# Performance work log

Measured on AMD Instinct MI355X. Metric: run time of the kernel, lower is better.

## Reference

```python
import jax, jax.numpy as jnp
import numpy as np

RETURN_SHAPE = (128, 128)


def dht2(x):
    # Discrete Hartley Transform over the spatial axes (2, 3):
    # H = Re(FFT) - Im(FFT). Unnormalized, matching scipy.fft default.
    f = jnp.fft.fftn(x, axes=(2, 3))
    return f.real - f.imag


def setup_inputs() -> dict:
    key = jax.random.key(0)
    x = jax.random.normal(key, (8, 64, 256, 256), dtype=jnp.float32)
    return {"x": x}


def reference(x) -> jnp.ndarray:
    # Spectral pooling: DHT -> center crop in frequency domain -> DHT.
    h_out, w_out = RETURN_SHAPE
    H, W = x.shape[2], x.shape[3]
    d = dht2(x)
    sh = (H - h_out) // 2
    sw = (W - w_out) // 2
    cropped = d[:, :, sh:sh + h_out, sw:sw + w_out]
    return dht2(cropped).astype(jnp.float32)
```

## Files before the change

kernel.cpp:

```cpp
#include <hip/hip_runtime.h>
#include <math.h>


typedef __attribute__((ext_vector_type(8))) short bfrag;
typedef __attribute__((ext_vector_type(4))) float ffrag;

#define PI2_256 0.0245436926061702597f
#define PI2_128 0.0490873852123405194f

__device__ __forceinline__ unsigned short f2bf(float f) {
    union { float f; unsigned int u; } v; v.f = f;
    unsigned int r = v.u + 0x7fffu + ((v.u >> 16) & 1u);
    return (unsigned short)(r >> 16);
}

__device__ __forceinline__ bfrag pack8(float4 a, float4 b) {
    bfrag r;
    r[0] = (short)f2bf(a.x); r[1] = (short)f2bf(a.y);
    r[2] = (short)f2bf(a.z); r[3] = (short)f2bf(a.w);
    r[4] = (short)f2bf(b.x); r[5] = (short)f2bf(b.y);
    r[6] = (short)f2bf(b.z); r[7] = (short)f2bf(b.w);
    return r;
}

__device__ __forceinline__ uint2 packlohi(ffrag a) {
    uint2 r;
    r.x = (unsigned int)f2bf(a[0]) | ((unsigned int)f2bf(a[1]) << 16);
    r.y = (unsigned int)f2bf(a[2]) | ((unsigned int)f2bf(a[3]) << 16);
    return r;
}

template<int NCOLS, int K, int NTH>
__device__ __forceinline__ void stageB(const unsigned short* __restrict__ src,
                                       unsigned short* __restrict__ Lb, int t)
{
    constexpr int CHUNKS = NCOLS * K / 8;
#pragma unroll
    for (int i = 0; i < CHUNKS / NTH; ++i) {
        const int o = (t + i * NTH) * 8;
        const int j = o / K;
        const int k = o - j * K;
        const uint4 v = *(const uint4*)(src + o);
        *(uint4*)&Lb[j * K + (((k >> 3) ^ (j & 7)) << 3)] = v;
    }
}

template<int K>
__device__ __forceinline__ bfrag ldsB(const unsigned short* __restrict__ Lb, int j, int k)
{
    return *(const bfrag*)&Lb[j * K + (((k >> 3) ^ (j & 7)) << 3)];
}

__global__ __launch_bounds__(256) void gen_tables(unsigned short* __restrict__ ws)
{
    const int id = blockIdx.x * 256 + threadIdx.x;
    {
        const int j = id >> 8, m = id & 255;
        const int mult = (j < 128) ? (64 + j) : (320 - j);
        const int idx = (mult * m) & 255;
        float s, c; sincosf((float)idx * PI2_256, &s, &c);
        ws[id] = f2bf(c + s);
    }
    {
        const int u = id >> 9, k = id & 511;
        const int up = 64 + u;
        float s, c, val;
        if (k < 256) { sincosf((float)((up * k) & 255) * PI2_256, &s, &c); val = c; }
        else         { sincosf((float)((up * (k - 256)) & 255) * PI2_256, &s, &c); val = s; }
        ws[65536 + id] = f2bf(val);
    }
    if (id < 32768) {
        {
            const int j = id >> 7, m = id & 127;
            const int mult = (j < 128) ? j : (256 - j);
            const int idx = (mult * m) & 127;
            float s, c; sincosf((float)idx * PI2_128, &s, &c);
            ws[131072 + id] = f2bf(c + s);
        }
        {
            const int u = id >> 8, k = id & 255;
            float s, c, val;
            if (k < 128) { sincosf((float)((u * k) & 127) * PI2_128, &s, &c); val = c; }
            else         { sincosf((float)((u * (k - 128)) & 127) * PI2_128, &s, &c); val = s; }
            ws[163840 + id] = f2bf(val);
        }
    }
}

__global__ __launch_bounds__(256, 1) void pass1(const float* __restrict__ X,
                                                const unsigned short* __restrict__ ws,
                                                unsigned short* __restrict__ Ct)
{
    __shared__ unsigned short Lb[128 * 256];

    const int t  = threadIdx.x;
    const int w  = t >> 6;
    const int ln = t & 15;
    const int q  = (t & 63) >> 4;
    const int img = blockIdx.x >> 1;
    const int h   = blockIdx.x & 1;

    stageB<128, 256, 256>(ws + h * 32768, Lb, t);
    __syncthreads();

    const float* __restrict__ Xi = X + (size_t)img * 65536;

    ffrag acc[4][8];
#pragma unroll
    for (int mt = 0; mt < 4; ++mt)
#pragma unroll
        for (int nt = 0; nt < 8; ++nt)
            acc[mt][nt] = (ffrag){0.f, 0.f, 0.f, 0.f};

#pragma unroll
    for (int kk = 0; kk < 8; ++kk) {
        const int k = kk * 32 + q * 8;
        bfrag A[4];
#pragma unroll
        for (int mt = 0; mt < 4; ++mt) {
            const float* xp = Xi + (size_t)(64 * w + 16 * mt + ln) * 256 + k;
            const float4 x0 = *(const float4*)xp;
            const float4 x1 = *(const float4*)(xp + 4);
            A[mt] = pack8(x0, x1);
        }
#pragma unroll
        for (int nt = 0; nt < 8; ++nt) {
            const bfrag B = ldsB<256>(Lb, nt * 16 + ln, k);
#pragma unroll
            for (int mt = 0; mt < 4; ++mt)
                acc[mt][nt] = __builtin_amdgcn_mfma_f32_16x16x32_bf16(A[mt], B, acc[mt][nt], 0, 0, 0);
        }
    }
#pragma unroll
    for (int mt = 0; mt < 4; ++mt) {
        unsigned short* __restrict__ Co = Ct + (size_t)img * 65536 + 64 * w + 16 * mt + 4 * q;
#pragma unroll
        for (int nt = 0; nt < 8; ++nt) {
            *(uint2*)&Co[(size_t)(128 * h + nt * 16 + ln) * 256] = packlohi(acc[mt][nt]);
        }
    }
}

__global__ __launch_bounds__(256, 2) void pass2(const unsigned short* __restrict__ Ct,
                                                const unsigned short* __restrict__ ws,
                                                unsigned short* __restrict__ Dc)
{
    __shared__ unsigned short Lb[64 * 512];

    const int t  = threadIdx.x;
    const int w  = t >> 6;
    const int ln = t & 15;
    const int q  = (t & 63) >> 4;
    const int img = blockIdx.x >> 1;
    const int hu  = blockIdx.x & 1;

    stageB<64, 512, 256>(ws + 65536 + hu * 32768, Lb, t);
    __syncthreads();

    const unsigned short* __restrict__ Abase = Ct + (size_t)img * 65536;

    ffrag acc[2][4];
#pragma unroll
    for (int mt = 0; mt < 2; ++mt)
#pragma unroll
        for (int nt = 0; nt < 4; ++nt)
            acc[mt][nt] = (ffrag){0.f, 0.f, 0.f, 0.f};

#pragma unroll
    for (int kh = 0; kh < 2; ++kh) {
#pragma unroll
        for (int kk = 0; kk < 8; ++kk) {
            const int k = kk * 32 + q * 8;
            const int kfull = kh * 256 + k;
            bfrag A[2];
#pragma unroll
            for (int mt = 0; mt < 2; ++mt) {
                const int v = 32 * w + 16 * mt + ln;
                A[mt] = *(const bfrag*)(Abase + (size_t)(v + kh * 128) * 256 + k);
            }
#pragma unroll
            for (int nt = 0; nt < 4; ++nt) {
                const bfrag B = ldsB<512>(Lb, nt * 16 + ln, kfull);
#pragma unroll
                for (int mt = 0; mt < 2; ++mt)
                    acc[mt][nt] = __builtin_amdgcn_mfma_f32_16x16x32_bf16(A[mt], B, acc[mt][nt], 0, 0, 0);
            }
        }
    }
#pragma unroll
    for (int mt = 0; mt < 2; ++mt) {
        unsigned short* __restrict__ Do = Dc + (size_t)img * 16384 + 32 * w + 16 * mt + 4 * q;
#pragma unroll
        for (int nt = 0; nt < 4; ++nt) {
            *(uint2*)&Do[(size_t)(64 * hu + nt * 16 + ln) * 128] = packlohi(acc[mt][nt]);
        }
    }
}

__global__ __launch_bounds__(256, 2) void pass3(const unsigned short* __restrict__ Dc,
                                                const unsigned short* __restrict__ ws,
                                                unsigned short* __restrict__ C3t)
{
    __shared__ unsigned short Lb[128 * 128];

    const int t  = threadIdx.x;
    const int w  = t >> 6;
    const int ln = t & 15;
    const int q  = (t & 63) >> 4;
    const int img = blockIdx.x >> 1;
    const int hj  = blockIdx.x & 1;

    stageB<128, 128, 256>(ws + 131072 + hj * 16384, Lb, t);
    __syncthreads();

    const unsigned short* __restrict__ Abase = Dc + (size_t)img * 16384;

    ffrag acc[2][8];
#pragma unroll
    for (int mt = 0; mt < 2; ++mt)
#pragma unroll
        for (int nt = 0; nt < 8; ++nt)
            acc[mt][nt] = (ffrag){0.f, 0.f, 0.f, 0.f};

#pragma unroll
    for (int kk = 0; kk < 4; ++kk) {
        const int k = kk * 32 + q * 8;
        bfrag A[2];
#pragma unroll
        for (int mt = 0; mt < 2; ++mt) {
            const int p = 32 * w + 16 * mt + ln;
            A[mt] = *(const bfrag*)(Abase + (size_t)p * 128 + k);
        }
#pragma unroll
        for (int nt = 0; nt < 8; ++nt) {
            const bfrag B = ldsB<128>(Lb, nt * 16 + ln, k);
#pragma unroll
            for (int mt = 0; mt < 2; ++mt)
                acc[mt][nt] = __builtin_amdgcn_mfma_f32_16x16x32_bf16(A[mt], B, acc[mt][nt], 0, 0, 0);
        }
    }
#pragma unroll
    for (int mt = 0; mt < 2; ++mt) {
        unsigned short* __restrict__ Co = C3t + (size_t)img * 32768 + 32 * w + 16 * mt + 4 * q;
#pragma unroll
        for (int nt = 0; nt < 8; ++nt) {
            *(uint2*)&Co[(size_t)(128 * hj + nt * 16 + ln) * 128] = packlohi(acc[mt][nt]);
        }
    }
}

__global__ __launch_bounds__(256, 2) void pass4(const unsigned short* __restrict__ C3t,
                                                const unsigned short* __restrict__ ws,
                                                float* __restrict__ out)
{
    __shared__ unsigned short Lb[64 * 256];

    const int t  = threadIdx.x;
    const int w  = t >> 6;
    const int ln = t & 15;
    const int q  = (t & 63) >> 4;
    const int img = blockIdx.x >> 1;
    const int hu  = blockIdx.x & 1;

    stageB<64, 256, 256>(ws + 163840 + hu * 16384, Lb, t);
    __syncthreads();

    const unsigned short* __restrict__ Abase = C3t + (size_t)img * 32768;

    ffrag acc[2][4];
#pragma unroll
    for (int mt = 0; mt < 2; ++mt)
#pragma unroll
        for (int nt = 0; nt < 4; ++nt)
            acc[mt][nt] = (ffrag){0.f, 0.f, 0.f, 0.f};

#pragma unroll
    for (int kh = 0; kh < 2; ++kh) {
#pragma unroll
        for (int kk = 0; kk < 4; ++kk) {
            const int k = kk * 32 + q * 8;
            const int kfull = kh * 128 + k;
            bfrag A[2];
#pragma unroll
            for (int mt = 0; mt < 2; ++mt) {
                const int v = 32 * w + 16 * mt + ln;
                A[mt] = *(const bfrag*)(Abase + (size_t)(v + kh * 128) * 128 + k);
            }
#pragma unroll
            for (int nt = 0; nt < 4; ++nt) {
                const bfrag B = ldsB<256>(Lb, nt * 16 + ln, kfull);
#pragma unroll
                for (int mt = 0; mt < 2; ++mt)
                    acc[mt][nt] = __builtin_amdgcn_mfma_f32_16x16x32_bf16(A[mt], B, acc[mt][nt], 0, 0, 0);
            }
        }
    }
#pragma unroll
    for (int mt = 0; mt < 2; ++mt) {
        float* __restrict__ G = out + (size_t)img * 16384 + 32 * w + 16 * mt + 4 * q;
#pragma unroll
        for (int nt = 0; nt < 4; ++nt) {
            float4 o4 = make_float4(acc[mt][nt][0], acc[mt][nt][1], acc[mt][nt][2], acc[mt][nt][3]);
            *(float4*)&G[(size_t)(64 * hu + nt * 16 + ln) * 128] = o4;
        }
    }
}

__global__ __launch_bounds__(512, 2) void stage1_old(const float* __restrict__ X,
                                                     const unsigned short* __restrict__ ws,
                                                     float* __restrict__ dc)
{
    __shared__ unsigned short PQt[128 * 512];

    const int t  = threadIdx.x;
    const int w  = t >> 6;
    const int ln = t & 15;
    const int q  = (t & 63) >> 4;
    const int img = blockIdx.x;

    const float* __restrict__ Xi = X + (size_t)img * 65536;
    const unsigned short* __restrict__ W1 = ws;
    const unsigned short* __restrict__ W2 = ws + 65536;

    {
        ffrag acc[2][16];
#pragma unroll
        for (int mt = 0; mt < 2; ++mt)
#pragma unroll
            for (int nt = 0; nt < 16; ++nt)
                acc[mt][nt] = (ffrag){0.f, 0.f, 0.f, 0.f};

        const int rowA0 = 32 * w;
        for (int kk = 0; kk < 8; ++kk) {
            const int k = kk * 32 + q * 8;
            bfrag A[2];
#pragma unroll
            for (int mt = 0; mt < 2; ++mt) {
                const float* xp = Xi + (size_t)(rowA0 + 16 * mt + ln) * 256 + k;
                const float4 x0 = *(const float4*)xp;
                const float4 x1 = *(const float4*)(xp + 4);
                A[mt] = pack8(x0, x1);
            }
#pragma unroll
            for (int nt = 0; nt < 16; ++nt) {
                const int j = nt * 16 + ln;
                const bfrag B = *(const bfrag*)(W1 + j * 256 + k);
#pragma unroll
                for (int mt = 0; mt < 2; ++mt)
                    acc[mt][nt] = __builtin_amdgcn_mfma_f32_16x16x32_bf16(A[mt], B, acc[mt][nt], 0, 0, 0);
            }
        }
#pragma unroll
        for (int mt = 0; mt < 2; ++mt) {
#pragma unroll
            for (int nt = 0; nt < 16; ++nt) {
                const int c  = nt * 16 + ln;
                const int v  = c & 127;
                const int kb = ((c < 128) ? 0 : 256) + rowA0 + 16 * mt + 4 * q;
                const uint2 lohi = packlohi(acc[mt][nt]);
                const int phys = v * 512 + (((kb >> 3) ^ (v & 7)) << 3) + (kb & 7);
                *(uint2*)&PQt[phys] = lohi;
            }
        }
    }
    __syncthreads();

    {
        ffrag acc[8];
#pragma unroll
        for (int nt = 0; nt < 8; ++nt) acc[nt] = (ffrag){0.f, 0.f, 0.f, 0.f};

        const int u0 = 16 * w;
        for (int kk = 0; kk < 16; ++kk) {
            const int k = kk * 32 + q * 8;
            const bfrag A = *(const bfrag*)(W2 + (size_t)(u0 + ln) * 512 + k);
#pragma unroll
            for (int nt = 0; nt < 8; ++nt) {
                const int v = nt * 16 + ln;
                const int g = (k >> 3) ^ (v & 7);
                const bfrag B = *(const bfrag*)&PQt[v * 512 + (g << 3)];
                acc[nt] = __builtin_amdgcn_mfma_f32_16x16x32_bf16(A, B, acc[nt], 0, 0, 0);
            }
        }
        float* __restrict__ D = dc + (size_t)img * 16384;
#pragma unroll
        for (int nt = 0; nt < 8; ++nt) {
#pragma unroll
            for (int r = 0; r < 4; ++r) {
                const int u = u0 + 4 * q + r;
                const int v = nt * 16 + ln;
                D[u * 128 + v] = acc[nt][r];
            }
        }
    }
}

__global__ __launch_bounds__(256, 2) void stage2_old(const unsigned short* __restrict__ ws,
                                                     float* __restrict__ io)
{
    __shared__ unsigned short Dcb[128 * 128];
    __shared__ unsigned short PQ2[64 * 256];

    const int t  = threadIdx.x;
    const int w  = t >> 6;
    const int ln = t & 15;
    const int q  = (t & 63) >> 4;
    const int img = blockIdx.x;

    float* __restrict__ G = io + (size_t)img * 16384;
    const unsigned short* __restrict__ W3 = ws + 131072;
    const unsigned short* __restrict__ W4 = ws + 163840;

    {
        const int p = t >> 1, half = t & 1;
        const float* src = G + p * 128 + half * 64;
#pragma unroll
        for (int g = 0; g < 8; ++g) {
            const float4 a = *(const float4*)(src + g * 8);
            const float4 b = *(const float4*)(src + g * 8 + 4);
            const int m0 = half * 64 + g * 8;
            const int gran = (m0 >> 3) ^ (p & 7);
            uint4 val;
            val.x = (unsigned int)f2bf(a.x) | ((unsigned int)f2bf(a.y) << 16);
            val.y = (unsigned int)f2bf(a.z) | ((unsigned int)f2bf(a.w) << 16);
            val.z = (unsigned int)f2bf(b.x) | ((unsigned int)f2bf(b.y) << 16);
            val.w = (unsigned int)f2bf(b.z) | ((unsigned int)f2bf(b.w) << 16);
            *(uint4*)&Dcb[p * 128 + gran * 8] = val;
        }
    }
    __syncthreads();

    for (int vh = 0; vh < 2; ++vh) {
        ffrag acc[2][8];
#pragma unroll
        for (int mt = 0; mt < 2; ++mt)
#pragma unroll
            for (int nt = 0; nt < 8; ++nt)
                acc[mt][nt] = (ffrag){0.f, 0.f, 0.f, 0.f};

        const int p0 = 32 * w;
        for (int kk = 0; kk < 4; ++kk) {
            const int k = kk * 32 + q * 8;
            bfrag A[2];
#pragma unroll
            for (int mt = 0; mt < 2; ++mt) {
                const int p = p0 + 16 * mt + ln;
                const int g = (k >> 3) ^ (p & 7);
                A[mt] = *(const bfrag*)&Dcb[p * 128 + g * 8];
            }
#pragma unroll
            for (int nt = 0; nt < 8; ++nt) {
                const int c = nt * 16 + ln;
                const int j = (c < 64) ? (64 * vh + c) : (128 + 64 * vh + (c - 64));
                const bfrag B = *(const bfrag*)(W3 + j * 128 + k);
#pragma unroll
                for (int mt = 0; mt < 2; ++mt)
                    acc[mt][nt] = __builtin_amdgcn_mfma_f32_16x16x32_bf16(A[mt], B, acc[mt][nt], 0, 0, 0);
            }
        }
        __syncthreads();
#pragma unroll
        for (int mt = 0; mt < 2; ++mt) {
#pragma unroll
            for (int nt = 0; nt < 8; ++nt) {
                const int c  = nt * 16 + ln;
                const int v  = c & 63;
                const int kb = ((c < 64) ? 0 : 128) + p0 + 16 * mt + 4 * q;
                const uint2 lohi = packlohi(acc[mt][nt]);
                const int phys = v * 256 + (((kb >> 3) ^ (v & 7)) << 3) + (kb & 7);
                *(uint2*)&PQ2[phys] = lohi;
            }
        }
        __syncthreads();

        ffrag o[2][4];
#pragma unroll
        for (int mt = 0; mt < 2; ++mt)
#pragma unroll
            for (int nt = 0; nt < 4; ++nt)
                o[mt][nt] = (ffrag){0.f, 0.f, 0.f, 0.f};

        const int u0 = 32 * w;
        for (int kk = 0; kk < 8; ++kk) {
            const int k = kk * 32 + q * 8;
            bfrag A[2];
#pragma unroll
            for (int mt = 0; mt < 2; ++mt)
                A[mt] = *(const bfrag*)(W4 + (size_t)(u0 + 16 * mt + ln) * 256 + k);
#pragma unroll
            for (int nt = 0; nt < 4; ++nt) {
                const int v = nt * 16 + ln;
                const int g = (k >> 3) ^ (v & 7);
                const bfrag B = *(const bfrag*)&PQ2[v * 256 + (g << 3)];
#pragma unroll
                for (int mt = 0; mt < 2; ++mt)
                    o[mt][nt] = __builtin_amdgcn_mfma_f32_16x16x32_bf16(A[mt], B, o[mt][nt], 0, 0, 0);
            }
        }
#pragma unroll
        for (int mt = 0; mt < 2; ++mt) {
#pragma unroll
            for (int nt = 0; nt < 4; ++nt) {
#pragma unroll
                for (int r = 0; r < 4; ++r) {
                    const int u = u0 + 16 * mt + 4 * q + r;
                    const int v = 64 * vh + nt * 16 + ln;
                    G[u * 128 + v] = o[mt][nt][r];
                }
            }
        }
    }
}

extern "C" void kernel_launch(void* const* d_in, const int* in_sizes, int n_in,
                              void* d_out, int out_size, void* d_ws, size_t ws_size,
                              hipStream_t stream)
{
    const float* x = (const float*)d_in[0];
    float* out = (float*)d_out;
    unsigned short* tw = (unsigned short*)d_ws;

    gen_tables<<<dim3(256), dim3(256), 0, stream>>>(tw);

    int G = 512;
    while (G > 1 && (size_t)163840 * (size_t)G + 393216 > ws_size) G >>= 1;

    if ((size_t)163840 * (size_t)G + 393216 <= ws_size) {
        unsigned short* regA  = tw + 196608;
        unsigned short* regDc = regA + (size_t)G * 65536;
        const int nchunks = 512 / G;
        for (int ci = 0; ci < nchunks; ++ci) {
            const float* xc = x + (size_t)ci * G * 65536;
            float* oc = out + (size_t)ci * G * 16384;
            pass1<<<dim3(2 * G), dim3(256), 0, stream>>>(xc, tw, regA);
            pass2<<<dim3(G * 2), dim3(256), 0, stream>>>(regA, tw, regDc);
            pass3<<<dim3(2 * G), dim3(256), 0, stream>>>(regDc, tw, regA);
            pass4<<<dim3(2 * G), dim3(256), 0, stream>>>(regA, tw, oc);
        }
    } else {
        stage1_old<<<dim3(512), dim3(512), 0, stream>>>(x, tw, out);
        stage2_old<<<dim3(512), dim3(256), 0, stream>>>(tw, out);
    }
}
```

Measured before the change: 289.1 us.

## Pre-convert input to bf16, split pass1 into quarter blocks, stage output via LDS

Adds a separate kernel that converts the fp32 input to bf16 once, so pass1 loads bf16 fragments directly instead of converting fp32 in its inner loop. pass1 now covers a quarter of the output columns per block with half the LDS, allowing two blocks per CU. Its results are transposed through swizzled LDS so the global stores are coalesced 16-byte writes. This costs an extra kernel launch plus a full bf16 write and read of the input, and the workspace requirement grows.

```diff
diff --git a/kernel.cpp b/kernel.cpp
--- a/kernel.cpp
+++ b/kernel.cpp
@@ -87,29 +87,42 @@
     }
 }
 
-__global__ __launch_bounds__(256, 1) void pass1(const float* __restrict__ X,
+__global__ __launch_bounds__(256) void convertX(const float* __restrict__ X,
+                                                unsigned short* __restrict__ Xb,
+                                                int n8)
+{
+    const int stride = gridDim.x * 256;
+    for (int i = blockIdx.x * 256 + threadIdx.x; i < n8; i += stride) {
+        const float4 a = *(const float4*)(X + (size_t)i * 8);
+        const float4 b = *(const float4*)(X + (size_t)i * 8 + 4);
+        const bfrag v = pack8(a, b);
+        *(uint4*)&Xb[(size_t)i * 8] = *(const uint4*)&v;
+    }
+}
+
+__global__ __launch_bounds__(256, 2) void pass1(const unsigned short* __restrict__ Xb,
                                                 const unsigned short* __restrict__ ws,
                                                 unsigned short* __restrict__ Ct)
 {
-    __shared__ unsigned short Lb[128 * 256];
+    __shared__ unsigned short Lb[64 * 256];
 
     const int t  = threadIdx.x;
     const int w  = t >> 6;
     const int ln = t & 15;
     const int q  = (t & 63) >> 4;
-    const int img = blockIdx.x >> 1;
-    const int h   = blockIdx.x & 1;
-
-    stageB<128, 256, 256>(ws + h * 32768, Lb, t);
-    __syncthreads();
-
-    const float* __restrict__ Xi = X + (size_t)img * 65536;
-
-    ffrag acc[4][8];
+    const int img = blockIdx.x >> 2;
+    const int h   = blockIdx.x & 3;
+
+    stageB<64, 256, 256>(ws + h * 16384, Lb, t);
+    __syncthreads();
+
+    const unsigned short* __restrict__ Xi = Xb + (size_t)img * 65536;
+
+    ffrag acc[4][4];
 #pragma unroll
     for (int mt = 0; mt < 4; ++mt)
 #pragma unroll
-        for (int nt = 0; nt < 8; ++nt)
+        for (int nt = 0; nt < 4; ++nt)
             acc[mt][nt] = (ffrag){0.f, 0.f, 0.f, 0.f};
 
 #pragma unroll
@@ -117,27 +130,37 @@
         const int k = kk * 32 + q * 8;
         bfrag A[4];
 #pragma unroll
-        for (int mt = 0; mt < 4; ++mt) {
-            const float* xp = Xi + (size_t)(64 * w + 16 * mt + ln) * 256 + k;
-            const float4 x0 = *(const float4*)xp;
-            const float4 x1 = *(const float4*)(xp + 4);
-            A[mt] = pack8(x0, x1);
-        }
-#pragma unroll
-        for (int nt = 0; nt < 8; ++nt) {
+        for (int mt = 0; mt < 4; ++mt)
+            A[mt] = *(const bfrag*)(Xi + (size_t)(64 * w + 16 * mt + ln) * 256 + k);
+#pragma unroll
+        for (int nt = 0; nt < 4; ++nt) {
             const bfrag B = ldsB<256>(Lb, nt * 16 + ln, k);
 #pragma unroll
             for (int mt = 0; mt < 4; ++mt)
                 acc[mt][nt] = __builtin_amdgcn_mfma_f32_16x16x32_bf16(A[mt], B, acc[mt][nt], 0, 0, 0);
         }
     }
+
+    __syncthreads();
 #pragma unroll
     for (int mt = 0; mt < 4; ++mt) {
-        unsigned short* __restrict__ Co = Ct + (size_t)img * 65536 + 64 * w + 16 * mt + 4 * q;
-#pragma unroll
-        for (int nt = 0; nt < 8; ++nt) {
-            *(uint2*)&Co[(size_t)(128 * h + nt * 16 + ln) * 256] = packlohi(acc[mt][nt]);
-        }
+#pragma unroll
+        for (int nt = 0; nt < 4; ++nt) {
+            const int cl = nt * 16 + ln;
+            const int n2 = 16 * w + 4 * mt + q;
+            const int phys = cl * 256 + (((n2 ^ ((cl & 7) << 3)) << 2));
+            *(uint2*)&Lb[phys] = packlohi(acc[mt][nt]);
+        }
+    }
+    __syncthreads();
+    unsigned short* __restrict__ Co = Ct + (size_t)img * 65536 + 16384 * h;
+#pragma unroll
+    for (int j = 0; j < 8; ++j) {
+        const int o   = (t + j * 256) * 8;
+        const int row = o >> 8;
+        const int ch  = (o & 255) >> 2;
+        const int phys = row * 256 + (((ch ^ ((row & 7) << 3)) << 2));
+        *(uint4*)&Co[o] = *(const uint4*)&Lb[phys];
     }
 }
 
@@ -523,18 +546,19 @@
     gen_tables<<<dim3(256), dim3(256), 0, stream>>>(tw);
 
     int G = 512;
-    while (G > 1 && (size_t)163840 * (size_t)G + 393216 > ws_size) G >>= 1;
-
-    if ((size_t)163840 * (size_t)G + 393216 <= ws_size) {
-        unsigned short* regA  = tw + 196608;
-        unsigned short* regDc = regA + (size_t)G * 65536;
+    while (G > 1 && (size_t)262144 * (size_t)G + 393216 > ws_size) G >>= 1;
+
+    if ((size_t)262144 * (size_t)G + 393216 <= ws_size) {
+        unsigned short* regA = tw + 196608;
+        unsigned short* regB = regA + (size_t)G * 65536;
         const int nchunks = 512 / G;
         for (int ci = 0; ci < nchunks; ++ci) {
             const float* xc = x + (size_t)ci * G * 65536;
             float* oc = out + (size_t)ci * G * 16384;
-            pass1<<<dim3(2 * G), dim3(256), 0, stream>>>(xc, tw, regA);
-            pass2<<<dim3(G * 2), dim3(256), 0, stream>>>(regA, tw, regDc);
-            pass3<<<dim3(2 * G), dim3(256), 0, stream>>>(regDc, tw, regA);
+            convertX<<<dim3(2048), dim3(256), 0, stream>>>(xc, regB, G * 8192);
+            pass1<<<dim3(4 * G), dim3(256), 0, stream>>>(regB, tw, regA);
+            pass2<<<dim3(2 * G), dim3(256), 0, stream>>>(regA, tw, regB);
+            pass3<<<dim3(2 * G), dim3(256), 0, stream>>>(regB, tw, regA);
             pass4<<<dim3(2 * G), dim3(256), 0, stream>>>(regA, tw, oc);
         }
     } else {
```

Result: slower. 323.0 us (+11.7%).
